# Performance work log

Measured on AMD Instinct MI355X. Metric: run time of the kernel, lower is better.

The kernel has to match this reference:

```python
import jax, jax.numpy as jnp
import numpy as np

N = 50000
E = 800000
C = 64
NEG_SLOPE = 0.2


def gat_conv(x, edge_index, W, att_src, att_dst, bias, heads, out_ch):
    """PyG GATConv forward (concat=True, add_self_loops=True).
    x: [N, in], edge_index: [2, E] (row0=src j, row1=dst i),
    W: [in, heads*out_ch], att_src/att_dst: [heads, out_ch], bias: [heads*out_ch].
    """
    n = x.shape[0]
    loop = jnp.arange(n, dtype=edge_index.dtype)
    src = jnp.concatenate([edge_index[0], loop])
    dst = jnp.concatenate([edge_index[1], loop])

    xl = (x @ W).reshape(n, heads, out_ch)            # [N, H, F]
    a_src = jnp.einsum('nhf,hf->nh', xl, att_src)      # [N, H]
    a_dst = jnp.einsum('nhf,hf->nh', xl, att_dst)      # [N, H]

    alpha = jax.nn.leaky_relu(a_src[src] + a_dst[dst], NEG_SLOPE)  # [E', H]
    # segment softmax over incoming edges of each destination node
    amax = jax.ops.segment_max(alpha, dst, num_segments=n)
    alpha = jnp.exp(alpha - amax[dst])
    denom = jax.ops.segment_sum(alpha, dst, num_segments=n)
    alpha = alpha / denom[dst]

    # gather source features, weight, scatter-add to destinations
    msg = xl[src] * alpha[:, :, None]                  # [E', H, F]
    out = jax.ops.segment_sum(msg, dst, num_segments=n)  # [N, H, F]
    return out.reshape(n, heads * out_ch) + bias


def setup_inputs() -> dict:
    key = jax.random.key(0)
    ks = jax.random.split(key, 12)
    x = jax.random.normal(ks[0], (N, C), dtype=jnp.float32)
    undirected = jax.random.randint(ks[1], (2, E), 0, N, dtype=jnp.int32)
    directed = jax.random.randint(ks[2], (2, E), 0, N, dtype=jnp.int32)

    s1 = 1.0 / np.sqrt(C)
    s2 = 1.0 / np.sqrt(2 * C)
    W1 = jax.random.normal(ks[3], (C, 2 * C), dtype=jnp.float32) * s1
    att_src1 = jax.random.normal(ks[4], (2, C), dtype=jnp.float32) * s1
    att_dst1 = jax.random.normal(ks[5], (2, C), dtype=jnp.float32) * s1
    b1 = jnp.zeros((2 * C,), dtype=jnp.float32)

    W2 = jax.random.normal(ks[6], (2 * C, 4 * C), dtype=jnp.float32) * s2
    att_src2 = jax.random.normal(ks[7], (2, 2 * C), dtype=jnp.float32) * s2
    att_dst2 = jax.random.normal(ks[8], (2, 2 * C), dtype=jnp.float32) * s2
    b2 = jnp.zeros((4 * C,), dtype=jnp.float32)

    return {
        'x': x,
        'undirected_edges_small': undirected,
        'directed_edges_small': directed,
        'W1': W1, 'att_src1': att_src1, 'att_dst1': att_dst1, 'b1': b1,
        'W2': W2, 'att_src2': att_src2, 'att_dst2': att_dst2, 'b2': b2,
    }


def reference(x, undirected_edges_small, directed_edges_small,
              W1, att_src1, att_dst1, b1,
              W2, att_src2, att_dst2, b2):
    h = gat_conv(x, undirected_edges_small, W1, att_src1, att_dst1, b1,
                 heads=2, out_ch=C)            # [N, 2C]
    out = gat_conv(h, directed_edges_small, W2, att_src2, att_dst2, b2,
                   heads=2, out_ch=2 * C)      # [N, 4C]
    return out
```

## Files before the change

### kernel.cpp

```cpp
#include <hip/hip_runtime.h>
#include <stdint.h>

#define N_NODES 50000
#define N_EDGES 800000
#define CAP 64
#define NBUCK 400
#define BSZ 125
#define BCAP 2816

typedef __attribute__((ext_vector_type(8))) short bf16x8;
typedef __attribute__((ext_vector_type(4))) float f32x4;

__device__ __forceinline__ float b2f_bits(unsigned int lo16) {
    union { unsigned int i; float f; } v; v.i = lo16 << 16; return v.f;
}
__device__ __forceinline__ unsigned short f2b(float f) {
    union { float f; unsigned int i; } v; v.f = f;
    unsigned int x = v.i;
    return (unsigned short)((x + 0x7fffu + ((x >> 16) & 1u)) >> 16);
}
__device__ __forceinline__ void split2(float v, unsigned short& h, unsigned short& l) {
    h = f2b(v);
    l = f2b(v - b2f_bits(h));
}
__device__ __forceinline__ void unpack8(const uint4 u, float* f) {
    f[0] = b2f_bits(u.x & 0xffffu); f[1] = b2f_bits(u.x >> 16);
    f[2] = b2f_bits(u.y & 0xffffu); f[3] = b2f_bits(u.y >> 16);
    f[4] = b2f_bits(u.z & 0xffffu); f[5] = b2f_bits(u.z >> 16);
    f[6] = b2f_bits(u.w & 0xffffu); f[7] = b2f_bits(u.w >> 16);
}
__device__ __forceinline__ void pack8hl(const float* v, uint4& H, uint4& L) {
    unsigned short h[8], l[8];
#pragma unroll
    for (int k = 0; k < 8; ++k) split2(v[k], h[k], l[k]);
    H.x = h[0] | ((unsigned)h[1] << 16); H.y = h[2] | ((unsigned)h[3] << 16);
    H.z = h[4] | ((unsigned)h[5] << 16); H.w = h[6] | ((unsigned)h[7] << 16);
    L.x = l[0] | ((unsigned)l[1] << 16); L.y = l[2] | ((unsigned)l[3] << 16);
    L.z = l[4] | ((unsigned)l[5] << 16); L.w = l[6] | ((unsigned)l[7] << 16);
}

__global__ __launch_bounds__(256) void proj_kernel(
    const float* __restrict__ W1, const float* __restrict__ as1, const float* __restrict__ ad1,
    const float* __restrict__ b1,
    const float* __restrict__ W2, const float* __restrict__ as2, const float* __restrict__ ad2,
    float* __restrict__ P1, float* __restrict__ q2, float* __restrict__ cs)
{
    __shared__ float p2[4 * 128];
    for (int i = threadIdx.x; i < 4 * 128; i += 256) {
        const int t = i >> 7, c = i & 127;
        const int h = t & 1;
        const float* att = (t < 2) ? as2 : ad2;
        float s = 0.f;
        for (int cc = 0; cc < 128; ++cc)
            s += att[h * 128 + cc] * W2[(size_t)c * 256 + h * 128 + cc];
        p2[i] = s;
    }
    {
        const int t = threadIdx.x >> 6, k = threadIdx.x & 63;
        const int h = t & 1;
        const float* att = (t < 2) ? as1 : ad1;
        float s = 0.f;
        for (int c = 0; c < 64; ++c)
            s += att[h * 64 + c] * W1[(size_t)k * 128 + h * 64 + c];
        P1[t * 64 + k] = s;
    }
    __syncthreads();
    for (int i = threadIdx.x; i < 4 * 128; i += 256) {
        const int t = i >> 7, j = i & 127;
        const int hc = j >> 6, k = j & 63;
        float s = 0.f;
        for (int c = 0; c < 64; ++c)
            s += W1[(size_t)k * 128 + hc * 64 + c] * p2[t * 128 + hc * 64 + c];
        q2[i] = s;
    }
    if (threadIdx.x < 4) {
        const int t = threadIdx.x;
        float s = 0.f;
        for (int c = 0; c < 128; ++c) s += b1[c] * p2[t * 128 + c];
        cs[t] = s;
    }
}

__global__ __launch_bounds__(256) void prep1_kernel(
    const float* __restrict__ X, const float* __restrict__ P1,
    unsigned short* __restrict__ Xh,
    float* __restrict__ a_src, float* __restrict__ a_dst, int n)
{
    const int node = (blockIdx.x * 256 + threadIdx.x) >> 4;
    const int sl = threadIdx.x & 15;
    if (node >= n) return;
    const float4 v = *(const float4*)(X + (size_t)node * 64 + sl * 4);
    ushort4 hv;
    hv.x = f2b(v.x); hv.y = f2b(v.y); hv.z = f2b(v.z); hv.w = f2b(v.w);
    *(ushort4*)(Xh + (size_t)node * 64 + sl * 4) = hv;
    float d[4];
#pragma unroll
    for (int t = 0; t < 4; ++t) {
        const float* pp = P1 + t * 64 + sl * 4;
        d[t] = v.x * pp[0] + v.y * pp[1] + v.z * pp[2] + v.w * pp[3];
    }
#pragma unroll
    for (int o = 1; o < 16; o <<= 1)
#pragma unroll
        for (int t = 0; t < 4; ++t) d[t] += __shfl_xor(d[t], o);
    if (sl == 0) {
        *(float2*)(a_src + node * 2) = make_float2(d[0], d[1]);
        *(float2*)(a_dst + node * 2) = make_float2(d[2], d[3]);
    }
}

__global__ __launch_bounds__(256) void prepW_kernel(
    const float* __restrict__ W1, const float* __restrict__ W2,
    unsigned short* __restrict__ w1h, unsigned short* __restrict__ w1l,
    unsigned short* __restrict__ w2h, unsigned short* __restrict__ w2l)
{
    const int bid = blockIdx.x;
    if (bid < 128) {
        const int i = bid * 256 + threadIdx.x;
        const int n = i >> 7, k = i & 127;
        unsigned short h, l;
        split2(W2[(size_t)k * 256 + n], h, l);
        w2h[i] = h; w2l[i] = l;
    } else {
        const int i = (bid - 128) * 256 + threadIdx.x;
        const int n = i >> 6, k = i & 63;
        unsigned short h, l;
        split2(W1[(size_t)k * 128 + n], h, l);
        w1h[i] = h; w1l[i] = l;
    }
}

__global__ __launch_bounds__(256) void bucket_kernel(
    const int* __restrict__ e1, const int* __restrict__ e2, int ne,
    int* __restrict__ gcur, unsigned int* __restrict__ stage)
{
    const int layer = blockIdx.x & 1;
    const int bslot = blockIdx.x >> 1;
    const int nbl = gridDim.x >> 1;
    const int* __restrict__ eix = layer ? e2 : e1;
    int* cur = gcur + layer * NBUCK;
    unsigned int* __restrict__ stg = stage + (size_t)layer * NBUCK * BCAP;

    __shared__ int cnt_lds[NBUCK];
    __shared__ int base_lds[NBUCK];
    constexpr int EPT = 16;
    constexpr int CHUNK = 256 * EPT;

    for (int base = bslot * CHUNK; base < ne; base += nbl * CHUNK) {
        for (int i = threadIdx.x; i < NBUCK; i += 256) cnt_lds[i] = 0;
        __syncthreads();

        unsigned int rec[EPT];
        int bk[EPT];
#pragma unroll
        for (int i = 0; i < EPT; ++i) {
            const int e = base + i * 256 + threadIdx.x;
            bk[i] = -1;
            if (e < ne) {
                const int s = eix[e];
                const int d = eix[ne + e];
                if ((unsigned)d < (unsigned)N_NODES) {
                    const int b = d / BSZ;
                    bk[i] = b;
                    rec[i] = (unsigned)s | ((unsigned)(d - b * BSZ) << 16);
                    atomicAdd(&cnt_lds[b], 1);
                }
            }
        }
        __syncthreads();
        for (int i = threadIdx.x; i < NBUCK; i += 256) {
            const int c = cnt_lds[i];
            base_lds[i] = c ? atomicAdd(&cur[i], c) : 0;
            cnt_lds[i] = 0;
        }
        __syncthreads();
#pragma unroll
        for (int i = 0; i < EPT; ++i) {
            if (bk[i] >= 0) {
                const int idx = base_lds[bk[i]] + atomicAdd(&cnt_lds[bk[i]], 1);
                if (idx < BCAP) stg[(size_t)bk[i] * BCAP + idx] = rec[i];
            }
        }
        __syncthreads();
    }
}

__global__ __launch_bounds__(256) void place_kernel(
    const unsigned int* __restrict__ stage, const int* __restrict__ gcur,
    int* __restrict__ cnt1, int* __restrict__ cnt2,
    int* __restrict__ ss1, int* __restrict__ ss2)
{
    const int layer = blockIdx.x & 1;
    const int bucket = blockIdx.x >> 1;
    int m = gcur[layer * NBUCK + bucket];
    m = m < BCAP ? m : BCAP;
    const unsigned int* __restrict__ stg =
        stage + ((size_t)(layer * NBUCK + bucket)) * BCAP;
    int* __restrict__ cnt = layer ? cnt2 : cnt1;
    int* __restrict__ ss  = layer ? ss2 : ss1;
    const int d0 = bucket * BSZ;

    __shared__ int c_lds[BSZ];
    __shared__ __align__(16) unsigned int img[BSZ * CAP];

    for (int i = threadIdx.x; i < BSZ; i += 256) c_lds[i] = 0;
    __syncthreads();

    for (int i = threadIdx.x; i < m; i += 256) {
        const unsigned int v = stg[i];
        const int dr = (int)(v >> 16);
        const int slot = atomicAdd(&c_lds[dr], 1);
        if (slot < CAP) img[dr * CAP + slot] = v & 0xffffu;
    }
    __syncthreads();

    uint4* dst4 = (uint4*)(ss + (size_t)d0 * CAP);
    const uint4* src4 = (const uint4*)img;
    constexpr int NV4 = BSZ * CAP / 4;
    for (int i = threadIdx.x; i < NV4; i += 256) dst4[i] = src4[i];
    for (int i = threadIdx.x; i < BSZ; i += 256) {
        const int c = c_lds[i];
        cnt[d0 + i] = c < CAP ? c : CAP;
    }
}

__global__ __launch_bounds__(256) void agg1_kernel(
    const unsigned short* __restrict__ XH, const float* __restrict__ X,
    const float* __restrict__ a_src, const float* __restrict__ a_dst,
    const int* __restrict__ cnt, const int* __restrict__ bins,
    unsigned short* __restrict__ AH, unsigned short* __restrict__ AL, int n)
{
    const int node = (blockIdx.x * 256 + threadIdx.x) >> 6;
    const int lane = threadIdx.x & 63;
    if (node >= n) return;
    const int hl = lane & 7;
    const int sub = lane >> 3;

    const int s = node * CAP;
    int deg = cnt[node]; deg = deg < CAP ? deg : CAP;
    const int e = s + deg;
    const float2 ad = *(const float2*)(a_dst + node * 2);

    float acc0[8] = {0.f,0.f,0.f,0.f,0.f,0.f,0.f,0.f};
    float acc1[8] = {0.f,0.f,0.f,0.f,0.f,0.f,0.f,0.f};
    float den0 = 0.f, den1 = 0.f;

    for (int p = s; p < e; p += 8) {
        const int pos = p + sub;
        const int pc = pos < e ? pos : e - 1;
        const int j = bins[pc];
        const float2 A = *(const float2*)(a_src + j * 2);
        const uint4 u = *(const uint4*)(XH + (size_t)j * 64 + hl * 8);
        float l0 = A.x + ad.x; l0 = l0 > 0.f ? l0 : 0.2f * l0;
        float l1 = A.y + ad.y; l1 = l1 > 0.f ? l1 : 0.2f * l1;
        float w0 = __expf(l0), w1 = __expf(l1);
        if (pos >= e) { w0 = 0.f; w1 = 0.f; }
        den0 += w0; den1 += w1;
        float f[8]; unpack8(u, f);
#pragma unroll
        for (int k = 0; k < 8; ++k) { acc0[k] += w0 * f[k]; acc1[k] += w1 * f[k]; }
    }
    if (sub == 0) {
        const float2 A = *(const float2*)(a_src + node * 2);
        const float4 va = *(const float4*)(X + (size_t)node * 64 + hl * 8);
        const float4 vb = *(const float4*)(X + (size_t)node * 64 + hl * 8 + 4);
        float l0 = A.x + ad.x; l0 = l0 > 0.f ? l0 : 0.2f * l0;
        float l1 = A.y + ad.y; l1 = l1 > 0.f ? l1 : 0.2f * l1;
        const float w0 = __expf(l0), w1 = __expf(l1);
        den0 += w0; den1 += w1;
        float f[8] = {va.x, va.y, va.z, va.w, vb.x, vb.y, vb.z, vb.w};
#pragma unroll
        for (int k = 0; k < 8; ++k) { acc0[k] += w0 * f[k]; acc1[k] += w1 * f[k]; }
    }
#pragma unroll
    for (int o = 8; o < 64; o <<= 1) {
        den0 += __shfl_xor(den0, o); den1 += __shfl_xor(den1, o);
#pragma unroll
        for (int k = 0; k < 8; ++k) {
            acc0[k] += __shfl_xor(acc0[k], o);
            acc1[k] += __shfl_xor(acc1[k], o);
        }
    }
    if (sub < 2) {
        const int head = sub;
        const float inv = 1.f / (head ? den1 : den0);
        float vv[8];
#pragma unroll
        for (int k = 0; k < 8; ++k) vv[k] = (head ? acc1[k] : acc0[k]) * inv;
        uint4 H, L;
        pack8hl(vv, H, L);
        const size_t off = (size_t)head * N_NODES * 64 + (size_t)node * 64 + hl * 8;
        *(uint4*)(AH + off) = H;
        *(uint4*)(AL + off) = L;
    }
}

__global__ __launch_bounds__(256) void agg2_kernel(
    const unsigned short* __restrict__ HH, const unsigned short* __restrict__ HL,
    const float* __restrict__ a_src, const float* __restrict__ a_dst,
    const float* __restrict__ cs,
    const int* __restrict__ cnt, const int* __restrict__ bins,
    unsigned short* __restrict__ AH, unsigned short* __restrict__ AL, int n)
{
    const int node = (blockIdx.x * 256 + threadIdx.x) >> 6;
    const int lane = threadIdx.x & 63;
    if (node >= n) return;
    const int hl = lane & 15;
    const int sub = lane >> 4;

    const float4 csv = *(const float4*)cs;
    const float C0 = csv.x + csv.z, C1 = csv.y + csv.w;

    const int s = node * CAP;
    int deg = cnt[node]; deg = deg < CAP ? deg : CAP;
    const int e = s + deg;
    const float2 ad = *(const float2*)(a_dst + node * 2);
    const float ad0 = ad.x + C0, ad1 = ad.y + C1;

    float acc0[8] = {0.f,0.f,0.f,0.f,0.f,0.f,0.f,0.f};
    float acc1[8] = {0.f,0.f,0.f,0.f,0.f,0.f,0.f,0.f};
    float den0 = 0.f, den1 = 0.f;

    for (int p = s; p < e; p += 4) {
        const int pos = p + sub;
        const int pc = pos < e ? pos : e - 1;
        const int j = bins[pc];
        const float2 A = *(const float2*)(a_src + j * 2);
        const uint4 u = *(const uint4*)(HH + (size_t)j * 128 + hl * 8);
        float l0 = A.x + ad0; l0 = l0 > 0.f ? l0 : 0.2f * l0;
        float l1 = A.y + ad1; l1 = l1 > 0.f ? l1 : 0.2f * l1;
        float w0 = __expf(l0), w1 = __expf(l1);
        if (pos >= e) { w0 = 0.f; w1 = 0.f; }
        den0 += w0; den1 += w1;
        float f[8]; unpack8(u, f);
#pragma unroll
        for (int k = 0; k < 8; ++k) { acc0[k] += w0 * f[k]; acc1[k] += w1 * f[k]; }
    }
    if (sub == 0) {
        const float2 A = *(const float2*)(a_src + node * 2);
        const uint4 uh = *(const uint4*)(HH + (size_t)node * 128 + hl * 8);
        const uint4 ul = *(const uint4*)(HL + (size_t)node * 128 + hl * 8);
        float l0 = A.x + ad0; l0 = l0 > 0.f ? l0 : 0.2f * l0;
        float l1 = A.y + ad1; l1 = l1 > 0.f ? l1 : 0.2f * l1;
        const float w0 = __expf(l0), w1 = __expf(l1);
        den0 += w0; den1 += w1;
        float fh[8], fl[8];
        unpack8(uh, fh); unpack8(ul, fl);
#pragma unroll
        for (int k = 0; k < 8; ++k) {
            const float f = fh[k] + fl[k];
            acc0[k] += w0 * f; acc1[k] += w1 * f;
        }
    }
#pragma unroll
    for (int o = 16; o < 64; o <<= 1) {
        den0 += __shfl_xor(den0, o); den1 += __shfl_xor(den1, o);
#pragma unroll
        for (int k = 0; k < 8; ++k) {
            acc0[k] += __shfl_xor(acc0[k], o);
            acc1[k] += __shfl_xor(acc1[k], o);
        }
    }
    if (sub < 2) {
        const int head = sub;
        const float inv = 1.f / (head ? den1 : den0);
        float vv[8];
#pragma unroll
        for (int k = 0; k < 8; ++k) vv[k] = (head ? acc1[k] : acc0[k]) * inv;
        uint4 H, L;
        pack8hl(vv, H, L);
        const size_t off = (size_t)head * N_NODES * 128 + (size_t)node * 128 + hl * 8;
        *(uint4*)(AH + off) = H;
        *(uint4*)(AL + off) = L;
    }
}

__global__ __launch_bounds__(512) void gemm_h_kernel(
    const unsigned short* __restrict__ AH, const unsigned short* __restrict__ AL,
    const unsigned short* __restrict__ WTh, const unsigned short* __restrict__ WTl,
    const float* __restrict__ b1, const float* __restrict__ q2,
    unsigned short* __restrict__ HH, unsigned short* __restrict__ HL,
    float* __restrict__ a_src2, float* __restrict__ a_dst2, int M)
{
    constexpr int K = 64, KC = 2;
    const int wave = threadIdx.x >> 6;
    const int lane = threadIdx.x & 63;
    const int head = wave >> 2;
    const int c0 = (wave & 3) * 16;
    const int lr = lane & 15;
    const int lk = (lane >> 4) * 8;
    const int colg = head * 64 + c0 + ((lane >> 4) << 2);
    const bool doAtt = (wave & 3) == 0;

    bf16x8 awh[KC], awl[KC];
    {
        const unsigned short* wr  = WTh + (size_t)(head * 64 + c0 + lr) * K + lk;
        const unsigned short* wr2 = WTl + (size_t)(head * 64 + c0 + lr) * K + lk;
#pragma unroll
        for (int c = 0; c < KC; ++c) {
            awh[c] = *(const bf16x8*)(wr + c * 32);
            awl[c] = *(const bf16x8*)(wr2 + c * 32);
        }
    }
    const float4 bias = *(const float4*)(b1 + colg);
    const unsigned short* XhB = AH + (size_t)head * M * 64;
    const unsigned short* XlB = AL + (size_t)head * M * 64;

    auto loadB = [&](bf16x8 (&bh)[KC], bf16x8 (&bl)[KC], int sidx) {
        const unsigned short* xr  = XhB + (size_t)(sidx * 16 + lr) * 64 + lk;
        const unsigned short* xr2 = XlB + (size_t)(sidx * 16 + lr) * 64 + lk;
#pragma unroll
        for (int c = 0; c < KC; ++c) {
            bh[c] = *(const bf16x8*)(xr + c * 32);
            bl[c] = *(const bf16x8*)(xr2 + c * 32);
        }
    };
    auto compute = [&](bf16x8 (&bh)[KC], bf16x8 (&bl)[KC], int sidx) {
        f32x4 acc = {0.f, 0.f, 0.f, 0.f};
#pragma unroll
        for (int c = 0; c < KC; ++c)
            acc = __builtin_amdgcn_mfma_f32_16x16x32_bf16(awh[c], bh[c], acc, 0, 0, 0);
#pragma unroll
        for (int c = 0; c < KC; ++c)
            acc = __builtin_amdgcn_mfma_f32_16x16x32_bf16(awh[c], bl[c], acc, 0, 0, 0);
#pragma unroll
        for (int c = 0; c < KC; ++c)
            acc = __builtin_amdgcn_mfma_f32_16x16x32_bf16(awl[c], bh[c], acc, 0, 0, 0);
        ushort4 hv, lv;
        split2(acc[0] + bias.x, hv.x, lv.x); split2(acc[1] + bias.y, hv.y, lv.y);
        split2(acc[2] + bias.z, hv.z, lv.z); split2(acc[3] + bias.w, hv.w, lv.w);
        const size_t o = (size_t)(sidx * 16 + lr) * 128 + colg;
        *(ushort4*)(HH + o) = hv;
        *(ushort4*)(HL + o) = lv;
        if (doAtt) {
            float P[4] = {0.f, 0.f, 0.f, 0.f};
#pragma unroll
            for (int c = 0; c < KC; ++c)
#pragma unroll
                for (int i = 0; i < 8; ++i) {
                    const float v = b2f_bits((unsigned short)bh[c][i])
                                  + b2f_bits((unsigned short)bl[c][i]);
                    const int kk = head * 64 + lk + c * 32 + i;
#pragma unroll
                    for (int t = 0; t < 4; ++t) P[t] += v * q2[t * 128 + kk];
                }
#pragma unroll
            for (int o2 = 16; o2 < 64; o2 <<= 1)
#pragma unroll
                for (int t = 0; t < 4; ++t) P[t] += __shfl_xor(P[t], o2);
            if (lane < 16) {
                const int m = sidx * 16 + lane;
                atomicAdd(&a_src2[m * 2 + 0], P[0]);
                atomicAdd(&a_src2[m * 2 + 1], P[1]);
                atomicAdd(&a_dst2[m * 2 + 0], P[2]);
                atomicAdd(&a_dst2[m * 2 + 1], P[3]);
            }
        }
    };

    const int NSTRIP = M / 16;
    const int nb = gridDim.x;
    int s = blockIdx.x;
    bf16x8 b0h[KC], b0l[KC], b1h_[KC], b1l_[KC];
    if (s < NSTRIP) loadB(b0h, b0l, s);
    while (s < NSTRIP) {
        const int sn = s + nb;
        if (sn < NSTRIP) loadB(b1h_, b1l_, sn);
        compute(b0h, b0l, s);
        if (sn >= NSTRIP) break;
        const int sn2 = sn + nb;
        if (sn2 < NSTRIP) loadB(b0h, b0l, sn2);
        compute(b1h_, b1l_, sn);
        s = sn2;
    }
}

__global__ __launch_bounds__(512) void gemm_out_kernel(
    const unsigned short* __restrict__ AH, const unsigned short* __restrict__ AL,
    const unsigned short* __restrict__ WTh, const unsigned short* __restrict__ WTl,
    const float* __restrict__ b2,
    float* __restrict__ OUT, int M)
{
    constexpr int K = 128, KC = 4, CT = 2;
    const int wave = threadIdx.x >> 6;
    const int lane = threadIdx.x & 63;
    const int head = wave >> 2;
    const int c0 = (wave & 3) * 32;
    const int lr = lane & 15;
    const int lk = (lane >> 4) * 8;

    bf16x8 awh[CT][KC], awl[CT][KC];
    float4 bias[CT];
    int colg[CT];
#pragma unroll
    for (int t = 0; t < CT; ++t) {
        const unsigned short* wr  = WTh + (size_t)(head * 128 + c0 + t * 16 + lr) * K + lk;
        const unsigned short* wr2 = WTl + (size_t)(head * 128 + c0 + t * 16 + lr) * K + lk;
#pragma unroll
        for (int c = 0; c < KC; ++c) {
            awh[t][c] = *(const bf16x8*)(wr + c * 32);
            awl[t][c] = *(const bf16x8*)(wr2 + c * 32);
        }
        colg[t] = head * 128 + c0 + t * 16 + ((lane >> 4) << 2);
        bias[t] = *(const float4*)(b2 + colg[t]);
    }
    const unsigned short* XhB = AH + (size_t)head * M * 128;
    const unsigned short* XlB = AL + (size_t)head * M * 128;

    auto loadB = [&](bf16x8 (&bh)[KC], bf16x8 (&bl)[KC], int sidx) {
        const unsigned short* xr  = XhB + (size_t)(sidx * 16 + lr) * 128 + lk;
        const unsigned short* xr2 = XlB + (size_t)(sidx * 16 + lr) * 128 + lk;
#pragma unroll
        for (int c = 0; c < KC; ++c) {
            bh[c] = *(const bf16x8*)(xr + c * 32);
            bl[c] = *(const bf16x8*)(xr2 + c * 32);
        }
    };
    auto compute = [&](bf16x8 (&bh)[KC], bf16x8 (&bl)[KC], int sidx) {
#pragma unroll
        for (int t = 0; t < CT; ++t) {
            f32x4 acc = {0.f, 0.f, 0.f, 0.f};
#pragma unroll
            for (int c = 0; c < KC; ++c)
                acc = __builtin_amdgcn_mfma_f32_16x16x32_bf16(awh[t][c], bh[c], acc, 0, 0, 0);
#pragma unroll
            for (int c = 0; c < KC; ++c)
                acc = __builtin_amdgcn_mfma_f32_16x16x32_bf16(awh[t][c], bl[c], acc, 0, 0, 0);
#pragma unroll
            for (int c = 0; c < KC; ++c)
                acc = __builtin_amdgcn_mfma_f32_16x16x32_bf16(awl[t][c], bh[c], acc, 0, 0, 0);
            float4 o;
            o.x = acc[0] + bias[t].x; o.y = acc[1] + bias[t].y;
            o.z = acc[2] + bias[t].z; o.w = acc[3] + bias[t].w;
            *(float4*)(OUT + (size_t)(sidx * 16 + lr) * 256 + colg[t]) = o;
        }
    };

    const int NSTRIP = M / 16;
    const int nb = gridDim.x;
    int s = blockIdx.x;
    bf16x8 b0h[KC], b0l[KC], b1h_[KC], b1l_[KC];
    if (s < NSTRIP) loadB(b0h, b0l, s);
    while (s < NSTRIP) {
        const int sn = s + nb;
        if (sn < NSTRIP) loadB(b1h_, b1l_, sn);
        compute(b0h, b0l, s);
        if (sn >= NSTRIP) break;
        const int sn2 = sn + nb;
        if (sn2 < NSTRIP) loadB(b0h, b0l, sn2);
        compute(b1h_, b1l_, sn);
        s = sn2;
    }
}

extern "C" void kernel_launch(void* const* d_in, const int* in_sizes, int n_in,
                              void* d_out, int out_size, void* d_ws, size_t ws_size,
                              hipStream_t stream)
{
    const int N = N_NODES, E = N_EDGES;

    const float* x   = (const float*)d_in[0];
    const int*   und = (const int*)d_in[1];
    const int*   dir = (const int*)d_in[2];
    const float* W1  = (const float*)d_in[3];
    const float* as1 = (const float*)d_in[4];
    const float* ad1 = (const float*)d_in[5];
    const float* b1  = (const float*)d_in[6];
    const float* W2  = (const float*)d_in[7];
    const float* as2 = (const float*)d_in[8];
    const float* ad2 = (const float*)d_in[9];
    const float* b2  = (const float*)d_in[10];

    char* p = (char*)d_ws;
    auto alloc = [&](size_t bytes) {
        char* r = p;
        p += (bytes + 255) & ~(size_t)255;
        return r;
    };
    unsigned short* agg2h = (unsigned short*)alloc((size_t)2 * N * 128 * 2);
    unsigned short* agg2l = (unsigned short*)alloc((size_t)2 * N * 128 * 2);
    unsigned short* hlbuf = (unsigned short*)alloc((size_t)N * 128 * 2);
    int*   ss1   = (int*)alloc((size_t)N * CAP * 4);
    int*   ss2   = (int*)alloc((size_t)N * CAP * 4);
    float* a_src1 = (float*)alloc((size_t)N * 2 * 4);
    float* a_dst1 = (float*)alloc((size_t)N * 2 * 4);
    float* att2buf = (float*)alloc((size_t)N * 4 * 4);
    int*   cnts  = (int*)alloc(((size_t)2 * N + 2 * NBUCK) * 4);
    unsigned short* w1th = (unsigned short*)alloc((size_t)128 * 64 * 2);
    unsigned short* w1tl = (unsigned short*)alloc((size_t)128 * 64 * 2);
    unsigned short* w2th = (unsigned short*)alloc((size_t)256 * 128 * 2);
    unsigned short* w2tl = (unsigned short*)alloc((size_t)256 * 128 * 2);
    float* P1d = (float*)alloc(4 * 64 * 4);
    float* q2d = (float*)alloc(4 * 128 * 4);
    float* csd = (float*)alloc(4 * 4);
    int* cnt1 = cnts, * cnt2 = cnts + N, * gcur = cnts + 2 * N;
    float* a_src2 = att2buf, * a_dst2 = att2buf + (size_t)N * 2;

    unsigned int* stage = (unsigned int*)agg2h;
    unsigned short* hhbuf = (unsigned short*)ss1;
    unsigned short* x1h   = (unsigned short*)d_out;
    unsigned short* agg1h = (unsigned short*)d_out + (size_t)N * 64;
    unsigned short* agg1l = (unsigned short*)d_out + (size_t)N * 64 + (size_t)N * 128;

    const int WB = (N * 64) / 256;

    proj_kernel<<<1, 256, 0, stream>>>(W1, as1, ad1, b1, W2, as2, ad2, P1d, q2d, csd);
    hipMemsetAsync(gcur, 0, (size_t)2 * NBUCK * 4, stream);
    hipMemsetAsync(att2buf, 0, (size_t)N * 4 * 4, stream);
    bucket_kernel<<<2 * 196, 256, 0, stream>>>(und, dir, E, gcur, stage);
    place_kernel<<<2 * NBUCK, 256, 0, stream>>>(stage, gcur, cnt1, cnt2, ss1, ss2);
    prep1_kernel<<<(N * 16) / 256, 256, 0, stream>>>(x, P1d, x1h, a_src1, a_dst1, N);
    prepW_kernel<<<160, 256, 0, stream>>>(W1, W2, w1th, w1tl, w2th, w2tl);

    agg1_kernel<<<WB, 256, 0, stream>>>(x1h, x, a_src1, a_dst1, cnt1, ss1, agg1h, agg1l, N);
    gemm_h_kernel<<<768, 512, 0, stream>>>(agg1h, agg1l, w1th, w1tl, b1, q2d,
                                           hhbuf, hlbuf, a_src2, a_dst2, N);

    agg2_kernel<<<WB, 256, 0, stream>>>(hhbuf, hlbuf, a_src2, a_dst2, csd,
                                        cnt2, ss2, agg2h, agg2l, N);
    gemm_out_kernel<<<512, 512, 0, stream>>>(agg2h, agg2l, w2th, w2tl, b2, (float*)d_out, N);
}
```

Baseline: 292.6 us.

## Compact CSR adjacency with 16-bit indices, prefetch gathers, fold log2e, merge prep kernels

Replaces the fixed-capacity 64-slot-per-node padded adjacency (int32) with a compact CSR layout: 16-bit source indices plus a packed offset/degree word per node, built by a two-pass count, prefix-sum and atomic base allocation in place_kernel. The aggregation loops software-pipeline the next neighbor's index, score and feature loads, and use exp2 with log2(e) pre-folded into the projection vectors. The memsets and the weight-split kernel are folded into existing kernels to cut launches. The compact layout cuts adjacency write and read traffic, but the 16-bit indices within a bucket rely on bucket-local packing, and the 7-bit degree field and larger offsets carry overflow assumptions.

```diff
diff --git a/kernel.cpp b/kernel.cpp
--- a/kernel.cpp
+++ b/kernel.cpp
@@ -7,6 +7,7 @@
 #define NBUCK 400
 #define BSZ 125
 #define BCAP 2816
+#define LOG2E 1.4426950408889634f
 
 typedef __attribute__((ext_vector_type(8))) short bf16x8;
 typedef __attribute__((ext_vector_type(4))) float f32x4;
@@ -43,8 +44,11 @@
     const float* __restrict__ W1, const float* __restrict__ as1, const float* __restrict__ ad1,
     const float* __restrict__ b1,
     const float* __restrict__ W2, const float* __restrict__ as2, const float* __restrict__ ad2,
-    float* __restrict__ P1, float* __restrict__ q2, float* __restrict__ cs)
-{
+    float* __restrict__ P1, float* __restrict__ q2, float* __restrict__ cs,
+    int* __restrict__ gcur)
+{
+    for (int i = threadIdx.x; i < 2 * NBUCK + 2; i += 256) gcur[i] = 0;
+
     __shared__ float p2[4 * 128];
     for (int i = threadIdx.x; i < 4 * 128; i += 256) {
         const int t = i >> 7, c = i & 127;
@@ -62,7 +66,7 @@
         float s = 0.f;
         for (int c = 0; c < 64; ++c)
             s += att[h * 64 + c] * W1[(size_t)k * 128 + h * 64 + c];
-        P1[t * 64 + k] = s;
+        P1[t * 64 + k] = s * LOG2E;
     }
     __syncthreads();
     for (int i = threadIdx.x; i < 4 * 128; i += 256) {
@@ -71,22 +75,45 @@
         float s = 0.f;
         for (int c = 0; c < 64; ++c)
             s += W1[(size_t)k * 128 + hc * 64 + c] * p2[t * 128 + hc * 64 + c];
-        q2[i] = s;
+        q2[i] = s * LOG2E;
     }
     if (threadIdx.x < 4) {
         const int t = threadIdx.x;
         float s = 0.f;
         for (int c = 0; c < 128; ++c) s += b1[c] * p2[t * 128 + c];
-        cs[t] = s;
+        cs[t] = s * LOG2E;
     }
 }
 
 __global__ __launch_bounds__(256) void prep1_kernel(
     const float* __restrict__ X, const float* __restrict__ P1,
+    const float* __restrict__ W1, const float* __restrict__ W2,
     unsigned short* __restrict__ Xh,
-    float* __restrict__ a_src, float* __restrict__ a_dst, int n)
-{
-    const int node = (blockIdx.x * 256 + threadIdx.x) >> 4;
+    float* __restrict__ a_src, float* __restrict__ a_dst,
+    unsigned short* __restrict__ w1h, unsigned short* __restrict__ w1l,
+    unsigned short* __restrict__ w2h, unsigned short* __restrict__ w2l,
+    float* __restrict__ att2buf, int n)
+{
+    const int bid = blockIdx.x;
+    if (bid < 128) {
+        const int i = bid * 256 + threadIdx.x;
+        const int nn = i >> 7, k = i & 127;
+        unsigned short h, l;
+        split2(W2[(size_t)k * 256 + nn], h, l);
+        w2h[i] = h; w2l[i] = l;
+        return;
+    }
+    if (bid < 160) {
+        const int i = (bid - 128) * 256 + threadIdx.x;
+        const int nn = i >> 6, k = i & 63;
+        unsigned short h, l;
+        split2(W1[(size_t)k * 128 + nn], h, l);
+        w1h[i] = h; w1l[i] = l;
+        return;
+    }
+    const int gid = (bid - 160) * 256 + threadIdx.x;
+    if (gid < n) ((float4*)att2buf)[gid] = make_float4(0.f, 0.f, 0.f, 0.f);
+    const int node = gid >> 4;
     const int sl = threadIdx.x & 15;
     if (node >= n) return;
     const float4 v = *(const float4*)(X + (size_t)node * 64 + sl * 4);
@@ -106,27 +133,6 @@
     if (sl == 0) {
         *(float2*)(a_src + node * 2) = make_float2(d[0], d[1]);
         *(float2*)(a_dst + node * 2) = make_float2(d[2], d[3]);
-    }
-}
-
-__global__ __launch_bounds__(256) void prepW_kernel(
-    const float* __restrict__ W1, const float* __restrict__ W2,
-    unsigned short* __restrict__ w1h, unsigned short* __restrict__ w1l,
-    unsigned short* __restrict__ w2h, unsigned short* __restrict__ w2l)
-{
-    const int bid = blockIdx.x;
-    if (bid < 128) {
-        const int i = bid * 256 + threadIdx.x;
-        const int n = i >> 7, k = i & 127;
-        unsigned short h, l;
-        split2(W2[(size_t)k * 256 + n], h, l);
-        w2h[i] = h; w2l[i] = l;
-    } else {
-        const int i = (bid - 128) * 256 + threadIdx.x;
-        const int n = i >> 6, k = i & 63;
-        unsigned short h, l;
-        split2(W1[(size_t)k * 128 + n], h, l);
-        w1h[i] = h; w1l[i] = l;
     }
 }
 
@@ -187,8 +193,9 @@
 
 __global__ __launch_bounds__(256) void place_kernel(
     const unsigned int* __restrict__ stage, const int* __restrict__ gcur,
-    int* __restrict__ cnt1, int* __restrict__ cnt2,
-    int* __restrict__ ss1, int* __restrict__ ss2)
+    int* __restrict__ gtot,
+    unsigned int* __restrict__ offs1, unsigned int* __restrict__ offs2,
+    unsigned short* __restrict__ ss1, unsigned short* __restrict__ ss2)
 {
     const int layer = blockIdx.x & 1;
     const int bucket = blockIdx.x >> 1;
@@ -196,38 +203,57 @@
     m = m < BCAP ? m : BCAP;
     const unsigned int* __restrict__ stg =
         stage + ((size_t)(layer * NBUCK + bucket)) * BCAP;
-    int* __restrict__ cnt = layer ? cnt2 : cnt1;
-    int* __restrict__ ss  = layer ? ss2 : ss1;
+    unsigned int* __restrict__ offs = layer ? offs2 : offs1;
+    unsigned short* __restrict__ ss = layer ? ss2 : ss1;
     const int d0 = bucket * BSZ;
 
     __shared__ int c_lds[BSZ];
-    __shared__ __align__(16) unsigned int img[BSZ * CAP];
+    __shared__ int pref[BSZ + 1];
+    __shared__ int baseSh;
+    __shared__ unsigned short img[BCAP];
 
     for (int i = threadIdx.x; i < BSZ; i += 256) c_lds[i] = 0;
+    __syncthreads();
+
+    for (int i = threadIdx.x; i < m; i += 256)
+        atomicAdd(&c_lds[stg[i] >> 16], 1);
+    __syncthreads();
+
+    if (threadIdx.x == 0) {
+        int run = 0;
+        for (int i = 0; i < BSZ; ++i) {
+            int c = c_lds[i]; c = c < CAP ? c : CAP;
+            pref[i] = run; run += c;
+        }
+        pref[BSZ] = run;
+        baseSh = atomicAdd(&gtot[layer], run);
+    }
+    __syncthreads();
+    const int base = baseSh;
+    for (int i = threadIdx.x; i < BSZ; i += 256) {
+        int c = c_lds[i]; c = c < CAP ? c : CAP;
+        offs[d0 + i] = ((unsigned)(base + pref[i]) << 7) | (unsigned)c;
+        c_lds[i] = 0;
+    }
     __syncthreads();
 
     for (int i = threadIdx.x; i < m; i += 256) {
         const unsigned int v = stg[i];
         const int dr = (int)(v >> 16);
         const int slot = atomicAdd(&c_lds[dr], 1);
-        if (slot < CAP) img[dr * CAP + slot] = v & 0xffffu;
+        if (slot < CAP) img[pref[dr] + slot] = (unsigned short)(v & 0xffffu);
     }
     __syncthreads();
 
-    uint4* dst4 = (uint4*)(ss + (size_t)d0 * CAP);
-    const uint4* src4 = (const uint4*)img;
-    constexpr int NV4 = BSZ * CAP / 4;
-    for (int i = threadIdx.x; i < NV4; i += 256) dst4[i] = src4[i];
-    for (int i = threadIdx.x; i < BSZ; i += 256) {
-        const int c = c_lds[i];
-        cnt[d0 + i] = c < CAP ? c : CAP;
-    }
+    unsigned short* out = ss + base;
+    const int tot = pref[BSZ];
+    for (int i = threadIdx.x; i < tot; i += 256) out[i] = img[i];
 }
 
 __global__ __launch_bounds__(256) void agg1_kernel(
     const unsigned short* __restrict__ XH, const float* __restrict__ X,
     const float* __restrict__ a_src, const float* __restrict__ a_dst,
-    const int* __restrict__ cnt, const int* __restrict__ bins,
+    const unsigned int* __restrict__ offs, const unsigned short* __restrict__ bins,
     unsigned short* __restrict__ AH, unsigned short* __restrict__ AL, int n)
 {
     const int node = (blockIdx.x * 256 + threadIdx.x) >> 6;
@@ -236,49 +262,72 @@
     const int hl = lane & 7;
     const int sub = lane >> 3;
 
-    const int s = node * CAP;
-    int deg = cnt[node]; deg = deg < CAP ? deg : CAP;
-    const int e = s + deg;
+    const unsigned o = offs[node];
+    const int start = (int)(o >> 7);
+    const int deg = (int)(o & 127);
+    const int e = start + deg;
     const float2 ad = *(const float2*)(a_dst + node * 2);
+
+    float2 As; float4 sva, svb;
+    if (sub == 0) {
+        As = *(const float2*)(a_src + node * 2);
+        sva = *(const float4*)(X + (size_t)node * 64 + hl * 8);
+        svb = *(const float4*)(X + (size_t)node * 64 + hl * 8 + 4);
+    }
 
     float acc0[8] = {0.f,0.f,0.f,0.f,0.f,0.f,0.f,0.f};
     float acc1[8] = {0.f,0.f,0.f,0.f,0.f,0.f,0.f,0.f};
     float den0 = 0.f, den1 = 0.f;
 
-    for (int p = s; p < e; p += 8) {
+    int p = start;
+    int jc = 0; float2 Ac = make_float2(0.f, 0.f); uint4 uc = make_uint4(0,0,0,0);
+    if (p < e) {
         const int pos = p + sub;
         const int pc = pos < e ? pos : e - 1;
-        const int j = bins[pc];
-        const float2 A = *(const float2*)(a_src + j * 2);
-        const uint4 u = *(const uint4*)(XH + (size_t)j * 64 + hl * 8);
-        float l0 = A.x + ad.x; l0 = l0 > 0.f ? l0 : 0.2f * l0;
-        float l1 = A.y + ad.y; l1 = l1 > 0.f ? l1 : 0.2f * l1;
-        float w0 = __expf(l0), w1 = __expf(l1);
-        if (pos >= e) { w0 = 0.f; w1 = 0.f; }
+        jc = bins[pc];
+        Ac = *(const float2*)(a_src + jc * 2);
+        uc = *(const uint4*)(XH + (size_t)jc * 64 + hl * 8);
+    }
+    while (p < e) {
+        const int pn = p + 8;
+        int jn = 0; float2 An; uint4 un;
+        const bool more = pn < e;
+        if (more) {
+            const int pos = pn + sub;
+            const int pc = pos < e ? pos : e - 1;
+            jn = bins[pc];
+            An = *(const float2*)(a_src + jn * 2);
+            un = *(const uint4*)(XH + (size_t)jn * 64 + hl * 8);
+        }
+        float l0 = Ac.x + ad.x; l0 = fmaxf(l0, 0.2f * l0);
+        float l1 = Ac.y + ad.y; l1 = fmaxf(l1, 0.2f * l1);
+        float w0 = __builtin_amdgcn_exp2f(l0);
+        float w1 = __builtin_amdgcn_exp2f(l1);
+        if (p + sub >= e) { w0 = 0.f; w1 = 0.f; }
         den0 += w0; den1 += w1;
-        float f[8]; unpack8(u, f);
+        float f[8]; unpack8(uc, f);
 #pragma unroll
         for (int k = 0; k < 8; ++k) { acc0[k] += w0 * f[k]; acc1[k] += w1 * f[k]; }
+        if (!more) break;
+        jc = jn; Ac = An; uc = un; p = pn;
     }
     if (sub == 0) {
-        const float2 A = *(const float2*)(a_src + node * 2);
-        const float4 va = *(const float4*)(X + (size_t)node * 64 + hl * 8);
-        const float4 vb = *(const float4*)(X + (size_t)node * 64 + hl * 8 + 4);
-        float l0 = A.x + ad.x; l0 = l0 > 0.f ? l0 : 0.2f * l0;
-        float l1 = A.y + ad.y; l1 = l1 > 0.f ? l1 : 0.2f * l1;
-        const float w0 = __expf(l0), w1 = __expf(l1);
+        float l0 = As.x + ad.x; l0 = fmaxf(l0, 0.2f * l0);
+        float l1 = As.y + ad.y; l1 = fmaxf(l1, 0.2f * l1);
+        const float w0 = __builtin_amdgcn_exp2f(l0);
+        const float w1 = __builtin_amdgcn_exp2f(l1);
         den0 += w0; den1 += w1;
-        float f[8] = {va.x, va.y, va.z, va.w, vb.x, vb.y, vb.z, vb.w};
+        float f[8] = {sva.x, sva.y, sva.z, sva.w, svb.x, svb.y, svb.z, svb.w};
 #pragma unroll
         for (int k = 0; k < 8; ++k) { acc0[k] += w0 * f[k]; acc1[k] += w1 * f[k]; }
     }
 #pragma unroll
-    for (int o = 8; o < 64; o <<= 1) {
-        den0 += __shfl_xor(den0, o); den1 += __shfl_xor(den1, o);
+    for (int o2 = 8; o2 < 64; o2 <<= 1) {
+        den0 += __shfl_xor(den0, o2); den1 += __shfl_xor(den1, o2);
 #pragma unroll
         for (int k = 0; k < 8; ++k) {
-            acc0[k] += __shfl_xor(acc0[k], o);
-            acc1[k] += __shfl_xor(acc1[k], o);
+            acc0[k] += __shfl_xor(acc0[k], o2);
+            acc1[k] += __shfl_xor(acc1[k], o2);
         }
     }
     if (sub < 2) {
@@ -299,7 +348,7 @@
     const unsigned short* __restrict__ HH, const unsigned short* __restrict__ HL,
     const float* __restrict__ a_src, const float* __restrict__ a_dst,
     const float* __restrict__ cs,
-    const int* __restrict__ cnt, const int* __restrict__ bins,
+    const unsigned int* __restrict__ offs, const unsigned short* __restrict__ bins,
     unsigned short* __restrict__ AH, unsigned short* __restrict__ AL, int n)
 {
     const int node = (blockIdx.x * 256 + threadIdx.x) >> 6;
@@ -311,41 +360,64 @@
     const float4 csv = *(const float4*)cs;
     const float C0 = csv.x + csv.z, C1 = csv.y + csv.w;
 
-    const int s = node * CAP;
-    int deg = cnt[node]; deg = deg < CAP ? deg : CAP;
-    const int e = s + deg;
+    const unsigned o = offs[node];
+    const int start = (int)(o >> 7);
+    const int deg = (int)(o & 127);
+    const int e = start + deg;
     const float2 ad = *(const float2*)(a_dst + node * 2);
     const float ad0 = ad.x + C0, ad1 = ad.y + C1;
+
+    float2 As; uint4 suh, sul;
+    if (sub == 0) {
+        As = *(const float2*)(a_src + node * 2);
+        suh = *(const uint4*)(HH + (size_t)node * 128 + hl * 8);
+        sul = *(const uint4*)(HL + (size_t)node * 128 + hl * 8);
+    }
 
     float acc0[8] = {0.f,0.f,0.f,0.f,0.f,0.f,0.f,0.f};
     float acc1[8] = {0.f,0.f,0.f,0.f,0.f,0.f,0.f,0.f};
     float den0 = 0.f, den1 = 0.f;
 
-    for (int p = s; p < e; p += 4) {
+    int p = start;
+    int jc = 0; float2 Ac = make_float2(0.f, 0.f); uint4 uc = make_uint4(0,0,0,0);
+    if (p < e) {
         const int pos = p + sub;
         const int pc = pos < e ? pos : e - 1;
-        const int j = bins[pc];
-        const float2 A = *(const float2*)(a_src + j * 2);
-        const uint4 u = *(const uint4*)(HH + (size_t)j * 128 + hl * 8);
-        float l0 = A.x + ad0; l0 = l0 > 0.f ? l0 : 0.2f * l0;
-        float l1 = A.y + ad1; l1 = l1 > 0.f ? l1 : 0.2f * l1;
-        float w0 = __expf(l0), w1 = __expf(l1);
-        if (pos >= e) { w0 = 0.f; w1 = 0.f; }
+        jc = bins[pc];
+        Ac = *(const float2*)(a_src + jc * 2);
+        uc = *(const uint4*)(HH + (size_t)jc * 128 + hl * 8);
+    }
+    while (p < e) {
+        const int pn = p + 4;
+        int jn = 0; float2 An; uint4 un;
+        const bool more = pn < e;
+        if (more) {
+            const int pos = pn + sub;
+            const int pc = pos < e ? pos : e - 1;
+            jn = bins[pc];
+            An = *(const float2*)(a_src + jn * 2);
+            un = *(const uint4*)(HH + (size_t)jn * 128 + hl * 8);
+        }
+        float l0 = Ac.x + ad0; l0 = fmaxf(l0, 0.2f * l0);
+        float l1 = Ac.y + ad1; l1 = fmaxf(l1, 0.2f * l1);
+        float w0 = __builtin_amdgcn_exp2f(l0);
+        float w1 = __builtin_amdgcn_exp2f(l1);
+        if (p + sub >= e) { w0 = 0.f; w1 = 0.f; }
         den0 += w0; den1 += w1;
-        float f[8]; unpack8(u, f);
+        float f[8]; unpack8(uc, f);
 #pragma unroll
         for (int k = 0; k < 8; ++k) { acc0[k] += w0 * f[k]; acc1[k] += w1 * f[k]; }
+        if (!more) break;
+        jc = jn; Ac = An; uc = un; p = pn;
     }
     if (sub == 0) {
-        const float2 A = *(const float2*)(a_src + node * 2);
-        const uint4 uh = *(const uint4*)(HH + (size_t)node * 128 + hl * 8);
-        const uint4 ul = *(const uint4*)(HL + (size_t)node * 128 + hl * 8);
-        float l0 = A.x + ad0; l0 = l0 > 0.f ? l0 : 0.2f * l0;
-        float l1 = A.y + ad1; l1 = l1 > 0.f ? l1 : 0.2f * l1;
-        const float w0 = __expf(l0), w1 = __expf(l1);
+        float l0 = As.x + ad0; l0 = fmaxf(l0, 0.2f * l0);
+        float l1 = As.y + ad1; l1 = fmaxf(l1, 0.2f * l1);
+        const float w0 = __builtin_amdgcn_exp2f(l0);
+        const float w1 = __builtin_amdgcn_exp2f(l1);
         den0 += w0; den1 += w1;
         float fh[8], fl[8];
-        unpack8(uh, fh); unpack8(ul, fl);
+        unpack8(suh, fh); unpack8(sul, fl);
 #pragma unroll
         for (int k = 0; k < 8; ++k) {
             const float f = fh[k] + fl[k];
@@ -353,12 +425,12 @@
         }
     }
 #pragma unroll
-    for (int o = 16; o < 64; o <<= 1) {
-        den0 += __shfl_xor(den0, o); den1 += __shfl_xor(den1, o);
+    for (int o2 = 16; o2 < 64; o2 <<= 1) {
+        den0 += __shfl_xor(den0, o2); den1 += __shfl_xor(den1, o2);
 #pragma unroll
         for (int k = 0; k < 8; ++k) {
-            acc0[k] += __shfl_xor(acc0[k], o);
-            acc1[k] += __shfl_xor(acc1[k], o);
+            acc0[k] += __shfl_xor(acc0[k], o2);
+            acc1[k] += __shfl_xor(acc1[k], o2);
         }
     }
     if (sub < 2) {
@@ -579,13 +651,16 @@
     };
     unsigned short* agg2h = (unsigned short*)alloc((size_t)2 * N * 128 * 2);
     unsigned short* agg2l = (unsigned short*)alloc((size_t)2 * N * 128 * 2);
+    unsigned short* hhbuf = (unsigned short*)alloc((size_t)N * 128 * 2);
     unsigned short* hlbuf = (unsigned short*)alloc((size_t)N * 128 * 2);
-    int*   ss1   = (int*)alloc((size_t)N * CAP * 4);
-    int*   ss2   = (int*)alloc((size_t)N * CAP * 4);
+    unsigned short* ss1   = (unsigned short*)alloc((size_t)E * 2);
+    unsigned short* ss2   = (unsigned short*)alloc((size_t)E * 2);
+    unsigned int* offs1 = (unsigned int*)alloc((size_t)N * 4);
+    unsigned int* offs2 = (unsigned int*)alloc((size_t)N * 4);
     float* a_src1 = (float*)alloc((size_t)N * 2 * 4);
     float* a_dst1 = (float*)alloc((size_t)N * 2 * 4);
     float* att2buf = (float*)alloc((size_t)N * 4 * 4);
-    int*   cnts  = (int*)alloc(((size_t)2 * N + 2 * NBUCK) * 4);
+    int*   gcur  = (int*)alloc(((size_t)2 * NBUCK + 2) * 4);
     unsigned short* w1th = (unsigned short*)alloc((size_t)128 * 64 * 2);
     unsigned short* w1tl = (unsigned short*)alloc((size_t)128 * 64 * 2);
     unsigned short* w2th = (unsigned short*)alloc((size_t)256 * 128 * 2);
@@ -593,30 +668,32 @@
     float* P1d = (float*)alloc(4 * 64 * 4);
     float* q2d = (float*)alloc(4 * 128 * 4);
     float* csd = (float*)alloc(4 * 4);
-    int* cnt1 = cnts, * cnt2 = cnts + N, * gcur = cnts + 2 * N;
+    int* gtot = gcur + 2 * NBUCK;
     float* a_src2 = att2buf, * a_dst2 = att2buf + (size_t)N * 2;
 
     unsigned int* stage = (unsigned int*)agg2h;
-    unsigned short* hhbuf = (unsigned short*)ss1;
     unsigned short* x1h   = (unsigned short*)d_out;
     unsigned short* agg1h = (unsigned short*)d_out + (size_t)N * 64;
     unsigned short* agg1l = (unsigned short*)d_out + (size_t)N * 64 + (size_t)N * 128;
 
     const int WB = (N * 64) / 256;
 
-    proj_kernel<<<1, 256, 0, stream>>>(W1, as1, ad1, b1, W2, as2, ad2, P1d, q2d, csd);
-    hipMemsetAsync(gcur, 0, (size_t)2 * NBUCK * 4, stream);
-    hipMemsetAsync(att2buf, 0, (size_t)N * 4 * 4, stream);
+    proj_kernel<<<1, 256, 0, stream>>>(W1, as1, ad1, b1, W2, as2, ad2,
+                                       P1d, q2d, csd, gcur);
     bucket_kernel<<<2 * 196, 256, 0, stream>>>(und, dir, E, gcur, stage);
-    place_kernel<<<2 * NBUCK, 256, 0, stream>>>(stage, gcur, cnt1, cnt2, ss1, ss2);
-    prep1_kernel<<<(N * 16) / 256, 256, 0, stream>>>(x, P1d, x1h, a_src1, a_dst1, N);
-    prepW_kernel<<<160, 256, 0, stream>>>(W1, W2, w1th, w1tl, w2th, w2tl);
-
-    agg1_kernel<<<WB, 256, 0, stream>>>(x1h, x, a_src1, a_dst1, cnt1, ss1, agg1h, agg1l, N);
+    place_kernel<<<2 * NBUCK, 256, 0, stream>>>(stage, gcur, gtot,
+                                                offs1, offs2, ss1, ss2);
+    prep1_kernel<<<160 + (N * 16) / 256, 256, 0, stream>>>(
+        x, P1d, W1, W2, x1h, a_src1, a_dst1,
+        w1th, w1tl, w2th, w2tl, att2buf, N);
+
+    agg1_kernel<<<WB, 256, 0, stream>>>(x1h, x, a_src1, a_dst1, offs1, ss1,
+                                        agg1h, agg1l, N);
     gemm_h_kernel<<<768, 512, 0, stream>>>(agg1h, agg1l, w1th, w1tl, b1, q2d,
                                            hhbuf, hlbuf, a_src2, a_dst2, N);
 
     agg2_kernel<<<WB, 256, 0, stream>>>(hhbuf, hlbuf, a_src2, a_dst2, csd,
-                                        cnt2, ss2, agg2h, agg2l, N);
-    gemm_out_kernel<<<512, 512, 0, stream>>>(agg2h, agg2l, w2th, w2tl, b2, (float*)d_out, N);
-}
+                                        offs2, ss2, agg2h, agg2l, N);
+    gemm_out_kernel<<<512, 512, 0, stream>>>(agg2h, agg2l, w2th, w2tl, b2,
+                                             (float*)d_out, N);
+}
```

Result: no change. 295.8 us (+1.1%).
